# Optimization experiments

Measured on AMD Instinct MI355X. Metric: run time of the kernel, lower is better.

## Reference

```python
import jax, jax.numpy as jnp
import numpy as np

B, T, C, H = 4, 1024, 1024, 16
HD = C // H
EPS = 1e-5


def _layernorm(x, w, b):
    mu = jnp.mean(x, axis=-1, keepdims=True)
    var = jnp.mean(jnp.square(x - mu), axis=-1, keepdims=True)
    return (x - mu) * jax.lax.rsqrt(var + EPS) * w + b


def setup_inputs() -> dict:
    key = jax.random.key(0)
    ks = jax.random.split(key, 10)
    s = 0.02
    return {
        "x": jax.random.normal(ks[0], (B, T, C), jnp.float32),
        "attention_mask": jnp.zeros((1, 1, T, T), jnp.float32),
        "ln1_w": jnp.ones((C,), jnp.float32),
        "ln1_b": jnp.zeros((C,), jnp.float32),
        "w_qkv": s * jax.random.normal(ks[1], (3 * C, C), jnp.float32),
        "b_qkv": jnp.zeros((3 * C,), jnp.float32),
        "w_o": s * jax.random.normal(ks[2], (C, C), jnp.float32),
        "b_o": jnp.zeros((C,), jnp.float32),
        "ln2_w": jnp.ones((C,), jnp.float32),
        "ln2_b": jnp.zeros((C,), jnp.float32),
        "w_fc": s * jax.random.normal(ks[3], (4 * C, C), jnp.float32),
        "b_fc": jnp.zeros((4 * C,), jnp.float32),
        "w_proj": s * jax.random.normal(ks[4], (C, 4 * C), jnp.float32),
        "b_proj": jnp.zeros((C,), jnp.float32),
    }


def reference(x, attention_mask, ln1_w, ln1_b, w_qkv, b_qkv, w_o, b_o,
              ln2_w, ln2_b, w_fc, b_fc, w_proj, b_proj):
    # --- self-attention on ln_1(x) ---
    h = _layernorm(x, ln1_w, ln1_b)
    qkv = h @ w_qkv.T + b_qkv                      # [B,T,3C]
    q, k, v = jnp.split(qkv, 3, axis=-1)
    q = q.reshape(B, T, H, HD).transpose(0, 2, 1, 3)  # [B,H,T,HD]
    k = k.reshape(B, T, H, HD).transpose(0, 2, 1, 3)
    v = v.reshape(B, T, H, HD).transpose(0, 2, 1, 3)
    att = jnp.einsum('bhqd,bhkd->bhqk', q, k) * (1.0 / np.sqrt(HD))
    att = att + attention_mask
    att_weights = jax.nn.softmax(att, axis=-1)     # [B,H,T,T]
    y = jnp.einsum('bhqk,bhkd->bhqd', att_weights, v)
    y = y.transpose(0, 2, 1, 3).reshape(B, T, C)
    y = y @ w_o.T + b_o
    x = x + y
    # --- MLP on ln_2(x), residual ---
    residual = x
    h2 = _layernorm(x, ln2_w, ln2_b)
    h2 = jax.nn.gelu(h2 @ w_fc.T + b_fc, approximate=False)
    h2 = h2 @ w_proj.T + b_proj
    x = residual + h2
    return (x, att_weights)
```

## Files before the change

### kernel.cpp

```cpp
#include <hip/hip_runtime.h>
#include <stdint.h>
#include <math.h>

typedef __attribute__((ext_vector_type(4))) float f32x4;
typedef __attribute__((ext_vector_type(8))) short s16x8;
typedef __attribute__((ext_vector_type(4))) unsigned short u16x4;

__device__ __forceinline__ unsigned short f2b(float x) {
    union { float f; uint32_t u; } v; v.f = x;
    uint32_t r = v.u + 0x7FFFu + ((v.u >> 16) & 1u);
    return (unsigned short)(r >> 16);
}
__device__ __forceinline__ float b2f(unsigned short u) {
    union { uint32_t u; float f; } v; v.u = (uint32_t)u << 16;
    return v.f;
}

__device__ __forceinline__ void gload16(const unsigned short* g, unsigned short* l) {
    __builtin_amdgcn_global_load_lds(
        (const __attribute__((address_space(1))) unsigned int*)(const void*)g,
        (__attribute__((address_space(3))) unsigned int*)(void*)l,
        16, 0, 0);
}

__device__ __forceinline__ float gelu_t(float u) {
    float z = 0.7978845608f * (u + 0.044715f * u * u * u);
    float ez = __expf(2.0f * z);
    float th = 1.0f - 2.0f / (ez + 1.0f);
    return 0.5f * u * (1.0f + th);
}

__global__ __launch_bounds__(256) void castln_kernel(
        const float* __restrict__ x, const float* __restrict__ lw,
        const float* __restrict__ lb, unsigned short* __restrict__ lout,
        const float* __restrict__ a, int na, const float* __restrict__ b, int nb,
        const float* __restrict__ c, int nc, const float* __restrict__ d, int nd,
        unsigned short* __restrict__ oa, unsigned short* __restrict__ ob,
        unsigned short* __restrict__ oc, unsigned short* __restrict__ od) {
    const int tid = threadIdx.x;
    if (blockIdx.x < 4096) {
        const long row = blockIdx.x;
        f32x4 v = *(const f32x4*)(x + row * 1024 + tid * 4);
        float s  = v[0] + v[1] + v[2] + v[3];
        float sq = v[0]*v[0] + v[1]*v[1] + v[2]*v[2] + v[3]*v[3];
        #pragma unroll
        for (int off = 32; off; off >>= 1) {
            s  += __shfl_xor(s, off);
            sq += __shfl_xor(sq, off);
        }
        __shared__ float red[8];
        if ((tid & 63) == 0) { red[tid >> 6] = s; red[4 + (tid >> 6)] = sq; }
        __syncthreads();
        s  = red[0] + red[1] + red[2] + red[3];
        sq = red[4] + red[5] + red[6] + red[7];
        float mu  = s * (1.0f / 1024.0f);
        float var = sq * (1.0f / 1024.0f) - mu * mu;
        float rs  = rsqrtf(var + 1e-5f);
        f32x4 wv = *(const f32x4*)(lw + tid * 4);
        f32x4 bv = *(const f32x4*)(lb + tid * 4);
        u16x4 o;
        #pragma unroll
        for (int j = 0; j < 4; ++j) o[j] = f2b((v[j] - mu) * rs * wv[j] + bv[j]);
        *(u16x4*)(lout + row * 1024 + tid * 4) = o;
    } else {
        int i = (blockIdx.x - 4096) * 256 + tid;
        const float* src; unsigned short* dst; int off;
        if (i < na)                { src = a; dst = oa; off = i; }
        else if (i < na+nb)        { src = b; dst = ob; off = i - na; }
        else if (i < na+nb+nc)     { src = c; dst = oc; off = i - na - nb; }
        else if (i < na+nb+nc+nd)  { src = d; dst = od; off = i - na - nb - nc; }
        else return;
        f32x4 v = ((const f32x4*)src)[off];
        u16x4 o;
        #pragma unroll
        for (int j = 0; j < 4; ++j) o[j] = f2b(v[j]);
        ((u16x4*)dst)[off] = o;
    }
}

__global__ __launch_bounds__(256) void ln_kernel(const float* __restrict__ x,
                                                 const float* __restrict__ w,
                                                 const float* __restrict__ b,
                                                 unsigned short* __restrict__ out) {
    const long row = blockIdx.x;
    const int tid = threadIdx.x;
    f32x4 v = *(const f32x4*)(x + row * 1024 + tid * 4);
    float s  = v[0] + v[1] + v[2] + v[3];
    float sq = v[0]*v[0] + v[1]*v[1] + v[2]*v[2] + v[3]*v[3];
    #pragma unroll
    for (int off = 32; off; off >>= 1) {
        s  += __shfl_xor(s, off);
        sq += __shfl_xor(sq, off);
    }
    __shared__ float red[8];
    if ((tid & 63) == 0) { red[tid >> 6] = s; red[4 + (tid >> 6)] = sq; }
    __syncthreads();
    s  = red[0] + red[1] + red[2] + red[3];
    sq = red[4] + red[5] + red[6] + red[7];
    float mu  = s * (1.0f / 1024.0f);
    float var = sq * (1.0f / 1024.0f) - mu * mu;
    float rs  = rsqrtf(var + 1e-5f);
    f32x4 wv = *(const f32x4*)(w + tid * 4);
    f32x4 bv = *(const f32x4*)(b + tid * 4);
    u16x4 o;
    #pragma unroll
    for (int j = 0; j < 4; ++j) o[j] = f2b((v[j] - mu) * rs * wv[j] + bv[j]);
    *(u16x4*)(out + row * 1024 + tid * 4) = o;
}

__global__ __launch_bounds__(256)
void attn2(const unsigned short* __restrict__ Qg,
           const unsigned short* __restrict__ Kg,
           const unsigned short* __restrict__ Vt,
           const float* __restrict__ mask,
           const float* __restrict__ psum,
           float* __restrict__ att,
           unsigned short* __restrict__ y) {
    __shared__ unsigned short Ks[2][64][72];
    __shared__ unsigned short Vs[2][64][72];
    __shared__ unsigned short Ps[4][16][72];
    __shared__ float invl_s[64];
    const int tid = threadIdx.x, lane = tid & 63, wid = tid >> 6;
    const int fr = lane & 15, fs = lane >> 4;
    const int bh = blockIdx.y, q0 = blockIdx.x * 64;

    if (tid < 64) {
        const float* p = psum + ((((long)bh << 10) + q0 + tid) << 4);
        f32x4 pa = *(const f32x4*)p,       pb = *(const f32x4*)(p + 4);
        f32x4 pc = *(const f32x4*)(p + 8), pd = *(const f32x4*)(p + 12);
        float s = (pa[0]+pa[1]+pa[2]+pa[3]) + (pb[0]+pb[1]+pb[2]+pb[3])
                + (pc[0]+pc[1]+pc[2]+pc[3]) + (pd[0]+pd[1]+pd[2]+pd[3]);
        invl_s[tid] = 1.0f / s;
    }

    const unsigned short* qp = Qg + ((long)bh << 16) + (long)(q0 + wid * 16 + fr) * 64 + fs * 8;
    const s16x8 aq0 = *(const s16x8*)qp;
    const s16x8 aq1 = *(const s16x8*)(qp + 32);

    const int srow = tid >> 2, scol = (tid & 3) * 16;
    const unsigned short* kbase = Kg + ((long)bh << 16) + (long)srow * 64 + scol;
    const unsigned short* vbase = Vt + ((long)bh << 16) + (long)srow * 1024 + scol;

    s16x8 k0a, k0b, v0a, v0b, k1a, k1b, v1a, v1b;
    k0a = *(const s16x8*)kbase;            k0b = *(const s16x8*)(kbase + 8);
    v0a = *(const s16x8*)vbase;            v0b = *(const s16x8*)(vbase + 8);
    k1a = *(const s16x8*)(kbase + 4096);   k1b = *(const s16x8*)(kbase + 4104);
    v1a = *(const s16x8*)(vbase + 64);     v1b = *(const s16x8*)(vbase + 72);

    f32x4 acc[4] = {};

#define AITER(KT, BUF, KA, KB, VA, VB)                                              \
    {                                                                               \
        *(s16x8*)&Ks[BUF][srow][scol]     = KA;                                     \
        *(s16x8*)&Ks[BUF][srow][scol + 8] = KB;                                     \
        *(s16x8*)&Vs[BUF][srow][scol]     = VA;                                     \
        *(s16x8*)&Vs[BUF][srow][scol + 8] = VB;                                     \
        __syncthreads();                                                            \
        if ((KT) + 2 < 16) {                                                        \
            const unsigned short* kp = kbase + (long)((KT) + 2) * 4096;             \
            const unsigned short* vp = vbase + ((KT) + 2) * 64;                     \
            KA = *(const s16x8*)kp;  KB = *(const s16x8*)(kp + 8);                  \
            VA = *(const s16x8*)vp;  VB = *(const s16x8*)(vp + 8);                  \
        }                                                                           \
        f32x4 s4[4];                                                                \
        _Pragma("unroll")                                                           \
        for (int n = 0; n < 4; ++n) {                                               \
            s16x8 b0 = *(const s16x8*)&Ks[BUF][n * 16 + fr][fs * 8];                \
            s16x8 b1 = *(const s16x8*)&Ks[BUF][n * 16 + fr][32 + fs * 8];           \
            f32x4 z = {};                                                           \
            z = __builtin_amdgcn_mfma_f32_16x16x32_bf16(aq0, b0, z, 0, 0, 0);       \
            z = __builtin_amdgcn_mfma_f32_16x16x32_bf16(aq1, b1, z, 0, 0, 0);       \
            s4[n] = z;                                                              \
        }                                                                           \
        _Pragma("unroll")                                                           \
        for (int r = 0; r < 4; ++r) {                                               \
            const long mb = ((long)(q0 + wid * 16 + fs * 4 + r) << 10) + (KT) * 64; \
            _Pragma("unroll")                                                       \
            for (int n = 0; n < 4; ++n) {                                           \
                float e = __expf(s4[n][r] + mask[mb + n * 16 + fr]);                \
                Ps[wid][fs * 4 + r][n * 16 + fr] = f2b(e);                          \
            }                                                                       \
        }                                                                           \
        {                                                                           \
            const float il = invl_s[srow];                                          \
            s16x8 p0 = *(const s16x8*)&Ps[wid][srow & 15][scol];                    \
            s16x8 p1 = *(const s16x8*)&Ps[wid][srow & 15][scol + 8];                \
            float* ap = att + ((long)bh << 20) + ((long)(q0 + srow) << 10)          \
                        + (KT) * 64 + scol;                                         \
            f32x4 o;                                                                \
            _Pragma("unroll") for (int j = 0; j < 4; ++j) o[j] = b2f((unsigned short)p0[j]) * il; \
            *(f32x4*)ap = o;                                                        \
            _Pragma("unroll") for (int j = 0; j < 4; ++j) o[j] = b2f((unsigned short)p0[4 + j]) * il; \
            *(f32x4*)(ap + 4) = o;                                                  \
            _Pragma("unroll") for (int j = 0; j < 4; ++j) o[j] = b2f((unsigned short)p1[j]) * il; \
            *(f32x4*)(ap + 8) = o;                                                  \
            _Pragma("unroll") for (int j = 0; j < 4; ++j) o[j] = b2f((unsigned short)p1[4 + j]) * il; \
            *(f32x4*)(ap + 12) = o;                                                 \
        }                                                                           \
        {                                                                           \
            s16x8 pa0 = *(const s16x8*)&Ps[wid][fr][fs * 8];                        \
            s16x8 pa1 = *(const s16x8*)&Ps[wid][fr][32 + fs * 8];                   \
            _Pragma("unroll")                                                       \
            for (int n = 0; n < 4; ++n) {                                           \
                s16x8 vb0 = *(const s16x8*)&Vs[BUF][n * 16 + fr][fs * 8];           \
                s16x8 vb1 = *(const s16x8*)&Vs[BUF][n * 16 + fr][32 + fs * 8];      \
                acc[n] = __builtin_amdgcn_mfma_f32_16x16x32_bf16(pa0, vb0, acc[n], 0, 0, 0); \
                acc[n] = __builtin_amdgcn_mfma_f32_16x16x32_bf16(pa1, vb1, acc[n], 0, 0, 0); \
            }                                                                       \
        }                                                                           \
    }

    for (int kt2 = 0; kt2 < 16; kt2 += 2) {
        AITER(kt2,     0, k0a, k0b, v0a, v0b);
        AITER(kt2 + 1, 1, k1a, k1b, v1a, v1b);
    }
#undef AITER

    const int bb = bh >> 4, hh = bh & 15;
    #pragma unroll
    for (int r = 0; r < 4; ++r) {
        const int q = q0 + wid * 16 + fs * 4 + r;
        const float il = invl_s[wid * 16 + fs * 4 + r];
        #pragma unroll
        for (int n = 0; n < 4; ++n)
            y[((long)(bb * 1024 + q) << 10) + hh * 64 + n * 16 + fr] = f2b(acc[n][r] * il);
    }
}

template <int BM, int BN, int EPI>
__global__ __launch_bounds__(256)
void gemm_bt(const unsigned short* __restrict__ A,
             const unsigned short* __restrict__ Bm,
             int K, int lda, int ldb, int ldc,
             long sAz, long sBz,
             const float* __restrict__ bias,
             const float* __restrict__ resid,
             float* __restrict__ outF,
             unsigned short* __restrict__ outB) {
    constexpr int WM = BM / 2, WN = BN / 2;
    constexpr int FM = WM / 16, FN = WN / 16;
    constexpr int NTA = BM / 64, NTB = BN / 64;
    constexpr int LOADS = NTA + NTB;
    constexpr int STR = 136;
    constexpr int STRF = 132;
    __shared__ unsigned short shm[3 * BM * 32 + 3 * BN * 32];
    unsigned short* ldsA = shm;
    unsigned short* ldsB = shm + 3 * BM * 32;

    const int tid  = threadIdx.x;
    const int lane = tid & 63;
    const int wid  = tid >> 6;
    const int wr   = wid >> 1, wc = wid & 1;
    const int bz   = blockIdx.z;
    const int row0 = blockIdx.x * BM;
    const int col0 = blockIdx.y * BN;

    const unsigned short* Ab = A + (long)bz * sAz + (long)row0 * lda;
    const unsigned short* Bb = Bm + (long)bz * sBz + (long)col0 * ldb;

    const int nt = K >> 5;
    f32x4 acc[FM][FN] = {};
    const int fr = lane & 15;
    const int fk = (lane >> 4) * 8;

#define STAGE(T, BUF)                                                              \
    {                                                                              \
        const int k0s = (T) << 5;                                                  \
        _Pragma("unroll")                                                          \
        for (int i = 0; i < NTA; ++i) {                                            \
            int e = i * 2048 + wid * 512 + lane * 8;                               \
            gload16(Ab + k0s + (long)(e >> 5) * lda + (e & 31),                    \
                    &ldsA[(BUF) * BM * 32 + i * 2048 + wid * 512]);                \
        }                                                                          \
        _Pragma("unroll")                                                          \
        for (int i = 0; i < NTB; ++i) {                                            \
            int e = i * 2048 + wid * 512 + lane * 8;                               \
            gload16(Bb + k0s + (long)(e >> 5) * ldb + (e & 31),                    \
                    &ldsB[(BUF) * BN * 32 + i * 2048 + wid * 512]);                \
        }                                                                          \
    }

    STAGE(0, 0);
    if (nt > 1) STAGE(1, 1);

    for (int t = 0; t < nt; ++t) {
        const int buf = t % 3;
        if (t + 1 < nt) {
            if constexpr (LOADS == 2)      asm volatile("s_waitcnt vmcnt(2)" ::: "memory");
            else if constexpr (LOADS == 3) asm volatile("s_waitcnt vmcnt(3)" ::: "memory");
            else                           asm volatile("s_waitcnt vmcnt(4)" ::: "memory");
        } else {
            asm volatile("s_waitcnt vmcnt(0)" ::: "memory");
        }
        __syncthreads();
        if (t + 2 < nt) STAGE(t + 2, (t + 2) % 3);

        s16x8 af[FM], bfr[FN];
        #pragma unroll
        for (int m = 0; m < FM; ++m)
            af[m] = *(const s16x8*)&ldsA[buf * BM * 32 + (wr * WM + m * 16 + fr) * 32 + fk];
        #pragma unroll
        for (int n = 0; n < FN; ++n)
            bfr[n] = *(const s16x8*)&ldsB[buf * BN * 32 + (wc * WN + n * 16 + fr) * 32 + fk];
        #pragma unroll
        for (int m = 0; m < FM; ++m)
            #pragma unroll
            for (int n = 0; n < FN; ++n)
                acc[m][n] = __builtin_amdgcn_mfma_f32_16x16x32_bf16(af[m], bfr[n], acc[m][n], 0, 0, 0);
    }
#undef STAGE

    const int cj = lane & 15;
    const int r0 = (lane >> 4) * 4;

    if constexpr (EPI == 5) {
        #pragma unroll
        for (int m = 0; m < FM; ++m) {
            #pragma unroll
            for (int r = 0; r < 4; ++r) {
                const int grow = row0 + wr * WM + m * 16 + r0 + r;
                float rs = 0.0f;
                #pragma unroll
                for (int n = 0; n < FN; ++n) {
                    const int gcol = col0 + wc * WN + n * 16 + cj;
                    rs += __expf(acc[m][n][r] + resid[((long)grow << 10) + gcol]);
                }
                rs += __shfl_xor(rs, 1); rs += __shfl_xor(rs, 2);
                rs += __shfl_xor(rs, 4); rs += __shfl_xor(rs, 8);
                if (cj == 0)
                    outF[((((long)bz << 10) + grow) << 4) + blockIdx.y * 2 + wc] = rs;
            }
        }
    } else if constexpr (EPI == 0) {
        const int seg = col0 >> 10;
        const int bb = row0 >> 10;
        __syncthreads();
        if (seg < 2) {
            #pragma unroll
            for (int m = 0; m < FM; ++m)
                #pragma unroll
                for (int n = 0; n < FN; ++n)
                    #pragma unroll
                    for (int r = 0; r < 4; ++r) {
                        const int prow = wr * WM + m * 16 + r0 + r;
                        const int pcol = wc * WN + n * 16 + cj;
                        float v = acc[m][n][r] + bias[col0 + pcol];
                        if (seg == 0) v *= 0.125f;
                        shm[prow * STR + pcol] = f2b(v);
                    }
            __syncthreads();
            #pragma unroll
            for (int j = 0; j < 8; ++j) {
                const int idx = j * 2048 + tid * 8;
                const int row = idx >> 7, c = idx & 127;
                s16x8 val = *(const s16x8*)&shm[row * STR + c];
                const int t = (row0 + row) & 1023;
                const int hh = ((col0 & 1023) >> 6) + (c >> 6);
                const int dd = c & 63;
                const long bh = bb * 16 + hh;
                *(s16x8*)(outB + (seg == 1 ? 4194304 : 0) + (bh << 16) + (t << 6) + dd) = val;
            }
        } else {
            #pragma unroll
            for (int m = 0; m < FM; ++m)
                #pragma unroll
                for (int n = 0; n < FN; ++n)
                    #pragma unroll
                    for (int r = 0; r < 4; ++r) {
                        const int prow = wr * WM + m * 16 + r0 + r;
                        const int pcol = wc * WN + n * 16 + cj;
                        shm[pcol * 144 + prow] = f2b(acc[m][n][r] + bias[col0 + pcol]);
                    }
            __syncthreads();
            #pragma unroll
            for (int j = 0; j < 8; ++j) {
                const int idx = j * 2048 + tid * 8;
                const int ddl = idx >> 7, tl = idx & 127;
                s16x8 val = *(const s16x8*)&shm[ddl * 144 + tl];
                const int hh = ((col0 & 1023) >> 6) + (ddl >> 6);
                const int dd = ddl & 63;
                const int t = (row0 & 1023) + tl;
                const long bh = bb * 16 + hh;
                *(s16x8*)(outB + 8388608 + (bh << 16) + (dd << 10) + t) = val;
            }
        }
    } else if constexpr (EPI == 4) {
        __syncthreads();
        #pragma unroll
        for (int m = 0; m < FM; ++m)
            #pragma unroll
            for (int n = 0; n < FN; ++n)
                #pragma unroll
                for (int r = 0; r < 4; ++r) {
                    const int prow = wr * WM + m * 16 + r0 + r;
                    const int pcol = wc * WN + n * 16 + cj;
                    float u = acc[m][n][r] + bias[col0 + pcol];
                    shm[prow * STR + pcol] = f2b(gelu_t(u));
                }
        __syncthreads();
        #pragma unroll
        for (int j = 0; j < 8; ++j) {
            const int idx = j * 2048 + tid * 8;
            const int row = idx >> 7, c = idx & 127;
            s16x8 val = *(const s16x8*)&shm[row * STR + c];
            *(s16x8*)(outB + (long)(row0 + row) * ldc + col0 + c) = val;
        }
    } else {
        float* shf = (float*)shm;
        __syncthreads();
        #pragma unroll
        for (int m = 0; m < FM; ++m)
            #pragma unroll
            for (int n = 0; n < FN; ++n)
                #pragma unroll
                for (int r = 0; r < 4; ++r) {
                    const int prow = wr * WM + m * 16 + r0 + r;
                    const int pcol = wc * WN + n * 16 + cj;
                    shf[prow * STRF + pcol] = acc[m][n][r];
                }
        __syncthreads();
        #pragma unroll
        for (int j = 0; j < (BM * BN / 1024); ++j) {
            const int idx = j * 1024 + tid * 4;
            const int row = idx >> 7, c = idx & 127;
            f32x4 v = *(const f32x4*)&shf[row * STRF + c];
            const long gbase = ((long)(row0 + row) << 10) + col0 + c;
            f32x4 bv = *(const f32x4*)(bias + col0 + c);
            f32x4 rv = *(const f32x4*)(resid + gbase);
            #pragma unroll
            for (int q = 0; q < 4; ++q) v[q] += bv[q] + rv[q];
            *(f32x4*)(outF + gbase) = v;
        }
    }
}

extern "C" void kernel_launch(void* const* d_in, const int* in_sizes, int n_in,
                              void* d_out, int out_size, void* d_ws, size_t ws_size,
                              hipStream_t stream) {
    (void)in_sizes; (void)n_in; (void)out_size; (void)ws_size;
    const float* x     = (const float*)d_in[0];
    const float* mask  = (const float*)d_in[1];
    const float* ln1w  = (const float*)d_in[2];
    const float* ln1b  = (const float*)d_in[3];
    const float* wqkv  = (const float*)d_in[4];
    const float* bqkv  = (const float*)d_in[5];
    const float* wo    = (const float*)d_in[6];
    const float* bo    = (const float*)d_in[7];
    const float* ln2w  = (const float*)d_in[8];
    const float* ln2b  = (const float*)d_in[9];
    const float* wfc   = (const float*)d_in[10];
    const float* bfc   = (const float*)d_in[11];
    const float* wproj = (const float*)d_in[12];
    const float* bproj = (const float*)d_in[13];

    float* outx = (float*)d_out;
    float* att  = (float*)d_out + 4194304;

    char* ws = (char*)d_ws;
    unsigned short* h_bf     = (unsigned short*)ws;  ws += (size_t)8  << 20;
    unsigned short* wqkv_bf  = (unsigned short*)ws;  ws += (size_t)6  << 20;
    unsigned short* wo_bf    = (unsigned short*)ws;  ws += (size_t)2  << 20;
    unsigned short* wfc_bf   = (unsigned short*)ws;  ws += (size_t)8  << 20;
    unsigned short* wproj_bf = (unsigned short*)ws;  ws += (size_t)8  << 20;
    unsigned short* q_bf     = (unsigned short*)ws;  ws += (size_t)24 << 20;
    unsigned short* k_bf     = q_bf + 4194304;
    unsigned short* vT_bf    = q_bf + 8388608;
    unsigned short* y_bf     = (unsigned short*)ws;  ws += (size_t)8  << 20;
    float*          x2       = (float*)ws;           ws += (size_t)16 << 20;
    unsigned short* gelu_bf  = (unsigned short*)ws;  ws += (size_t)32 << 20;
    float*          psum     = (float*)ws;           ws += (size_t)4  << 20;

    castln_kernel<<<16384, 256, 0, stream>>>(
        x, ln1w, ln1b, h_bf,
        wqkv, 786432, wo, 262144, wfc, 1048576, wproj, 1048576,
        wqkv_bf, wo_bf, wfc_bf, wproj_bf);

    gemm_bt<128, 128, 0><<<dim3(32, 24, 1), 256, 0, stream>>>(
        h_bf, wqkv_bf, 1024, 1024, 1024, 0, 0, 0,
        bqkv, nullptr, nullptr, q_bf);

    gemm_bt<128, 128, 5><<<dim3(8, 8, 64), 256, 0, stream>>>(
        q_bf, k_bf, 64, 64, 64, 0, 65536, 65536,
        nullptr, mask, psum, nullptr);

    attn2<<<dim3(16, 64), 256, 0, stream>>>(
        q_bf, k_bf, vT_bf, mask, psum, att, y_bf);

    gemm_bt<64, 128, 3><<<dim3(64, 8, 1), 256, 0, stream>>>(
        y_bf, wo_bf, 1024, 1024, 1024, 1024, 0, 0,
        bo, x, x2, nullptr);

    ln_kernel<<<4096, 256, 0, stream>>>(x2, ln2w, ln2b, h_bf);

    gemm_bt<128, 128, 4><<<dim3(32, 32, 1), 256, 0, stream>>>(
        h_bf, wfc_bf, 1024, 1024, 1024, 4096, 0, 0,
        bfc, nullptr, nullptr, gelu_bf);

    gemm_bt<64, 128, 3><<<dim3(64, 8, 1), 256, 0, stream>>>(
        gelu_bf, wproj_bf, 4096, 4096, 4096, 1024, 0, 0,
        bproj, x2, outx, nullptr);
}
```

Measured before the change: 394.0 us.

## Replace FC GEMM with 256x256-tile 8-wave kernel using triple-buffered async LDS loads

Adds a dedicated kernel for the MLP up-projection GEMM with fused GELU. It uses 256x256 output tiles, 512 threads (8 waves), and a three-stage global-to-LDS pipeline with explicit vmcnt waits and loads split across two half-iterations. The aim is more operand reuse per LDS byte and better overlap of memory with MFMA work than the generic 128x128 kernel. The cost is 96KB of LDS and many accumulator registers per thread, which lowers occupancy, and only 256 blocks, which may leave CUs under-filled. The old GELU epilogue branch of the generic GEMM is removed.

```diff
diff --git a/kernel.cpp b/kernel.cpp
--- a/kernel.cpp
+++ b/kernel.cpp
@@ -227,6 +227,97 @@
     }
 }
 
+__global__ __launch_bounds__(512, 2)
+void gemm8p_fc(const unsigned short* __restrict__ A,
+               const unsigned short* __restrict__ Bm,
+               const float* __restrict__ bias,
+               unsigned short* __restrict__ outB) {
+    __shared__ unsigned short shm8[49152];
+    const int tid = threadIdx.x, lane = tid & 63, wid = tid >> 6;
+    const int wr = wid >> 2, wcn = wid & 3;
+    const int fr = lane & 15, kg = lane >> 4;
+    const int row0 = blockIdx.x * 256, col0 = blockIdx.y * 256;
+    const unsigned short* Ab = A + (long)row0 * 1024;
+    const unsigned short* Bb = Bm + (long)col0 * 1024;
+
+    const int sr = tid >> 2, sc = (tid & 3) * 8;
+#define STG_A(T, H) gload16(Ab + (long)(sr + (H) * 128) * 1024 + ((T) << 5) + sc, \
+                            &shm8[((T) % 3) * 8192 + (H) * 4096 + wid * 512 + lane * 8])
+#define STG_B(T, H) gload16(Bb + (long)(sr + (H) * 128) * 1024 + ((T) << 5) + sc, \
+                            &shm8[24576 + ((T) % 3) * 8192 + (H) * 4096 + wid * 512 + lane * 8])
+
+    STG_A(0, 0); STG_A(0, 1); STG_B(0, 0); STG_B(0, 1);
+    STG_A(1, 0); STG_A(1, 1); STG_B(1, 0); STG_B(1, 1);
+
+    f32x4 acc[8][4] = {};
+
+    for (int t = 0; t < 32; ++t) {
+        const int buf = t % 3;
+        const unsigned short* As = &shm8[buf * 8192];
+        const unsigned short* Bs = &shm8[24576 + buf * 8192];
+        if (t < 31) asm volatile("s_waitcnt vmcnt(4)" ::: "memory");
+        else        asm volatile("s_waitcnt vmcnt(0)" ::: "memory");
+        __syncthreads();
+
+        s16x8 bb[4], af[4];
+        #pragma unroll
+        for (int n = 0; n < 4; ++n)
+            bb[n] = *(const s16x8*)&Bs[(wcn * 64 + n * 16 + fr) * 32 + kg * 8];
+        #pragma unroll
+        for (int m = 0; m < 4; ++m)
+            af[m] = *(const s16x8*)&As[(wr * 128 + m * 16 + fr) * 32 + kg * 8];
+        if (t + 2 < 32) { STG_A(t + 2, 0); STG_A(t + 2, 1); }
+        __builtin_amdgcn_s_setprio(1);
+        #pragma unroll
+        for (int m = 0; m < 4; ++m)
+            #pragma unroll
+            for (int n = 0; n < 4; ++n)
+                acc[m][n] = __builtin_amdgcn_mfma_f32_16x16x32_bf16(af[m], bb[n], acc[m][n], 0, 0, 0);
+        __builtin_amdgcn_s_setprio(0);
+        __syncthreads();
+
+        #pragma unroll
+        for (int m = 0; m < 4; ++m)
+            af[m] = *(const s16x8*)&As[(wr * 128 + (m + 4) * 16 + fr) * 32 + kg * 8];
+        if (t + 2 < 32) { STG_B(t + 2, 0); STG_B(t + 2, 1); }
+        __builtin_amdgcn_s_setprio(1);
+        #pragma unroll
+        for (int m = 0; m < 4; ++m)
+            #pragma unroll
+            for (int n = 0; n < 4; ++n)
+                acc[m + 4][n] = __builtin_amdgcn_mfma_f32_16x16x32_bf16(af[m], bb[n], acc[m + 4][n], 0, 0, 0);
+        __builtin_amdgcn_s_setprio(0);
+    }
+#undef STG_A
+#undef STG_B
+
+    #pragma unroll
+    for (int h = 0; h < 2; ++h) {
+        __syncthreads();
+        if (wr == h) {
+            #pragma unroll
+            for (int m = 0; m < 8; ++m)
+                #pragma unroll
+                for (int n = 0; n < 4; ++n)
+                    #pragma unroll
+                    for (int r = 0; r < 4; ++r) {
+                        const int prow = m * 16 + kg * 4 + r;
+                        const int pcol = wcn * 64 + n * 16 + fr;
+                        float u = acc[m][n][r] + bias[col0 + pcol];
+                        shm8[prow * 264 + pcol] = f2b(gelu_t(u));
+                    }
+        }
+        __syncthreads();
+        #pragma unroll
+        for (int j = 0; j < 8; ++j) {
+            const int idx = j * 4096 + tid * 8;
+            const int row = idx >> 8, c = idx & 255;
+            s16x8 val = *(const s16x8*)&shm8[row * 264 + c];
+            *(s16x8*)(outB + (long)(row0 + h * 128 + row) * 4096 + col0 + c) = val;
+        }
+    }
+}
+
 template <int BM, int BN, int EPI>
 __global__ __launch_bounds__(256)
 void gemm_bt(const unsigned short* __restrict__ A,
@@ -384,27 +475,6 @@
                 *(s16x8*)(outB + 8388608 + (bh << 16) + (dd << 10) + t) = val;
             }
         }
-    } else if constexpr (EPI == 4) {
-        __syncthreads();
-        #pragma unroll
-        for (int m = 0; m < FM; ++m)
-            #pragma unroll
-            for (int n = 0; n < FN; ++n)
-                #pragma unroll
-                for (int r = 0; r < 4; ++r) {
-                    const int prow = wr * WM + m * 16 + r0 + r;
-                    const int pcol = wc * WN + n * 16 + cj;
-                    float u = acc[m][n][r] + bias[col0 + pcol];
-                    shm[prow * STR + pcol] = f2b(gelu_t(u));
-                }
-        __syncthreads();
-        #pragma unroll
-        for (int j = 0; j < 8; ++j) {
-            const int idx = j * 2048 + tid * 8;
-            const int row = idx >> 7, c = idx & 127;
-            s16x8 val = *(const s16x8*)&shm[row * STR + c];
-            *(s16x8*)(outB + (long)(row0 + row) * ldc + col0 + c) = val;
-        }
     } else {
         float* shf = (float*)shm;
         __syncthreads();
@@ -492,9 +562,7 @@
 
     ln_kernel<<<4096, 256, 0, stream>>>(x2, ln2w, ln2b, h_bf);
 
-    gemm_bt<128, 128, 4><<<dim3(32, 32, 1), 256, 0, stream>>>(
-        h_bf, wfc_bf, 1024, 1024, 1024, 4096, 0, 0,
-        bfc, nullptr, nullptr, gelu_bf);
+    gemm8p_fc<<<dim3(16, 16), 512, 0, stream>>>(h_bf, wfc_bf, bfc, gelu_bf);
 
     gemm_bt<64, 128, 3><<<dim3(64, 8, 1), 256, 0, stream>>>(
         gelu_bf, wproj_bf, 4096, 4096, 4096, 1024, 0, 0,
```

After: 394.1 us. No clear change (+0.0%).

## Fuse softmax row-sum pass into attention kernel, dropping separate QK GEMM launch

Applied to the files above, without the earlier changes.

Removes the separate gemm_bt EPI=5 launch that computed the exp row sums into a psum buffer. The attention kernel now makes a first pass over K tiles, recomputing QK^T with MFMA and accumulating exp(score+mask) per row to get 1/l before the main pass. This saves a kernel launch and the psum write and read, but QK^T is now computed twice inside one kernel, so the attention kernel does more work per block.

```diff
diff --git a/kernel.cpp b/kernel.cpp
--- a/kernel.cpp
+++ b/kernel.cpp
@@ -109,13 +109,12 @@
 }
 
 __global__ __launch_bounds__(256)
-void attn2(const unsigned short* __restrict__ Qg,
-           const unsigned short* __restrict__ Kg,
-           const unsigned short* __restrict__ Vt,
-           const float* __restrict__ mask,
-           const float* __restrict__ psum,
-           float* __restrict__ att,
-           unsigned short* __restrict__ y) {
+void attn_all(const unsigned short* __restrict__ Qg,
+              const unsigned short* __restrict__ Kg,
+              const unsigned short* __restrict__ Vt,
+              const float* __restrict__ mask,
+              float* __restrict__ att,
+              unsigned short* __restrict__ y) {
     __shared__ unsigned short Ks[2][64][72];
     __shared__ unsigned short Vs[2][64][72];
     __shared__ unsigned short Ps[4][16][72];
@@ -124,15 +123,6 @@
     const int fr = lane & 15, fs = lane >> 4;
     const int bh = blockIdx.y, q0 = blockIdx.x * 64;
 
-    if (tid < 64) {
-        const float* p = psum + ((((long)bh << 10) + q0 + tid) << 4);
-        f32x4 pa = *(const f32x4*)p,       pb = *(const f32x4*)(p + 4);
-        f32x4 pc = *(const f32x4*)(p + 8), pd = *(const f32x4*)(p + 12);
-        float s = (pa[0]+pa[1]+pa[2]+pa[3]) + (pb[0]+pb[1]+pb[2]+pb[3])
-                + (pc[0]+pc[1]+pc[2]+pc[3]) + (pd[0]+pd[1]+pd[2]+pd[3]);
-        invl_s[tid] = 1.0f / s;
-    }
-
     const unsigned short* qp = Qg + ((long)bh << 16) + (long)(q0 + wid * 16 + fr) * 64 + fs * 8;
     const s16x8 aq0 = *(const s16x8*)qp;
     const s16x8 aq1 = *(const s16x8*)(qp + 32);
@@ -140,6 +130,50 @@
     const int srow = tid >> 2, scol = (tid & 3) * 16;
     const unsigned short* kbase = Kg + ((long)bh << 16) + (long)srow * 64 + scol;
     const unsigned short* vbase = Vt + ((long)bh << 16) + (long)srow * 1024 + scol;
+
+    float rs4[4] = {0.0f, 0.0f, 0.0f, 0.0f};
+    {
+        s16x8 ka0 = *(const s16x8*)kbase,          kc0 = *(const s16x8*)(kbase + 8);
+        s16x8 ka1 = *(const s16x8*)(kbase + 4096), kc1 = *(const s16x8*)(kbase + 4104);
+
+#define PITER(KT, BUF, KA, KB)                                                      \
+        {                                                                           \
+            *(s16x8*)&Ks[BUF][srow][scol]     = KA;                                 \
+            *(s16x8*)&Ks[BUF][srow][scol + 8] = KB;                                 \
+            __syncthreads();                                                        \
+            if ((KT) + 2 < 16) {                                                    \
+                const unsigned short* kp = kbase + (long)((KT) + 2) * 4096;         \
+                KA = *(const s16x8*)kp;  KB = *(const s16x8*)(kp + 8);              \
+            }                                                                       \
+            _Pragma("unroll")                                                       \
+            for (int n = 0; n < 4; ++n) {                                           \
+                s16x8 b0 = *(const s16x8*)&Ks[BUF][n * 16 + fr][fs * 8];            \
+                s16x8 b1 = *(const s16x8*)&Ks[BUF][n * 16 + fr][32 + fs * 8];       \
+                f32x4 z = {};                                                       \
+                z = __builtin_amdgcn_mfma_f32_16x16x32_bf16(aq0, b0, z, 0, 0, 0);   \
+                z = __builtin_amdgcn_mfma_f32_16x16x32_bf16(aq1, b1, z, 0, 0, 0);   \
+                _Pragma("unroll")                                                   \
+                for (int r = 0; r < 4; ++r) {                                       \
+                    const long mb = ((long)(q0 + wid * 16 + fs * 4 + r) << 10)      \
+                                    + (KT) * 64;                                    \
+                    rs4[r] += __expf(z[r] + mask[mb + n * 16 + fr]);                \
+                }                                                                   \
+            }                                                                       \
+        }
+
+        for (int kt2 = 0; kt2 < 16; kt2 += 2) {
+            PITER(kt2,     0, ka0, kc0);
+            PITER(kt2 + 1, 1, ka1, kc1);
+        }
+#undef PITER
+    }
+    #pragma unroll
+    for (int r = 0; r < 4; ++r) {
+        float t = rs4[r];
+        t += __shfl_xor(t, 1); t += __shfl_xor(t, 2);
+        t += __shfl_xor(t, 4); t += __shfl_xor(t, 8);
+        if (fr == 0) invl_s[wid * 16 + fs * 4 + r] = 1.0f / t;
+    }
 
     s16x8 k0a, k0b, v0a, v0b, k1a, k1b, v1a, v1b;
     k0a = *(const s16x8*)kbase;            k0b = *(const s16x8*)(kbase + 8);
@@ -313,25 +347,7 @@
     const int cj = lane & 15;
     const int r0 = (lane >> 4) * 4;
 
-    if constexpr (EPI == 5) {
-        #pragma unroll
-        for (int m = 0; m < FM; ++m) {
-            #pragma unroll
-            for (int r = 0; r < 4; ++r) {
-                const int grow = row0 + wr * WM + m * 16 + r0 + r;
-                float rs = 0.0f;
-                #pragma unroll
-                for (int n = 0; n < FN; ++n) {
-                    const int gcol = col0 + wc * WN + n * 16 + cj;
-                    rs += __expf(acc[m][n][r] + resid[((long)grow << 10) + gcol]);
-                }
-                rs += __shfl_xor(rs, 1); rs += __shfl_xor(rs, 2);
-                rs += __shfl_xor(rs, 4); rs += __shfl_xor(rs, 8);
-                if (cj == 0)
-                    outF[((((long)bz << 10) + grow) << 4) + blockIdx.y * 2 + wc] = rs;
-            }
-        }
-    } else if constexpr (EPI == 0) {
+    if constexpr (EPI == 0) {
         const int seg = col0 >> 10;
         const int bb = row0 >> 10;
         __syncthreads();
@@ -468,7 +484,6 @@
     unsigned short* y_bf     = (unsigned short*)ws;  ws += (size_t)8  << 20;
     float*          x2       = (float*)ws;           ws += (size_t)16 << 20;
     unsigned short* gelu_bf  = (unsigned short*)ws;  ws += (size_t)32 << 20;
-    float*          psum     = (float*)ws;           ws += (size_t)4  << 20;
 
     castln_kernel<<<16384, 256, 0, stream>>>(
         x, ln1w, ln1b, h_bf,
@@ -479,12 +494,8 @@
         h_bf, wqkv_bf, 1024, 1024, 1024, 0, 0, 0,
         bqkv, nullptr, nullptr, q_bf);
 
-    gemm_bt<128, 128, 5><<<dim3(8, 8, 64), 256, 0, stream>>>(
-        q_bf, k_bf, 64, 64, 64, 0, 65536, 65536,
-        nullptr, mask, psum, nullptr);
-
-    attn2<<<dim3(16, 64), 256, 0, stream>>>(
-        q_bf, k_bf, vT_bf, mask, psum, att, y_bf);
+    attn_all<<<dim3(16, 64), 256, 0, stream>>>(
+        q_bf, k_bf, vT_bf, mask, att, y_bf);
 
     gemm_bt<64, 128, 3><<<dim3(64, 8, 1), 256, 0, stream>>>(
         y_bf, wo_bf, 1024, 1024, 1024, 1024, 0, 0,
```

Result: faster. 361.1 us, median of 2 (-8.4%).
